# Kernel optimization log

Hardware: AMD Instinct MI355X
Metric: run time of the kernel (lower is better)

Reference implementation:

```python
import jax, jax.numpy as jnp
import numpy as np

EMBED_DIM = 1024
NUM_HEADS = 16
HEAD_DIM = EMBED_DIM // NUM_HEADS


def setup_inputs() -> dict:
    key = jax.random.key(0)
    ks = jax.random.split(key, 9)
    B, S, E = 4, 2048, EMBED_DIM
    # xavier_uniform bound for square [E, E] weights
    bound = float(np.sqrt(6.0 / (E + E)))
    def w(k):
        return jax.random.uniform(k, (E, E), jnp.float32, -bound, bound)
    return {
        "x": jax.random.normal(ks[0], (B, S, E), jnp.float32),
        "Wq": w(ks[1]), "bq": jnp.zeros((E,), jnp.float32),
        "Wk": w(ks[2]), "bk": jnp.zeros((E,), jnp.float32),
        "Wv": w(ks[3]), "bv": jnp.zeros((E,), jnp.float32),
        "Wo": w(ks[4]), "bo": jnp.zeros((E,), jnp.float32),
    }


def reference(x, Wq, bq, Wk, bk, Wv, bv, Wo, bo):
    B, S, E = x.shape
    H, D = NUM_HEADS, HEAD_DIM
    # Linear projections (torch Linear: x @ W.T + b)
    q = (x @ Wq.T + bq).reshape(B, S, H, D)
    k = (x @ Wk.T + bk).reshape(B, S, H, D)
    v = (x @ Wv.T + bv).reshape(B, S, H, D)
    # per-head scaled dot-product attention (vectorized over heads)
    scores = jnp.einsum("bqhd,bkhd->bhqk", q, k) / jnp.sqrt(jnp.float32(D))
    attn = jax.nn.softmax(scores, axis=-1)
    o = jnp.einsum("bhqk,bkhd->bqhd", attn, v).reshape(B, S, E)
    return o @ Wo.T + bo
```

## Files before the change

kernel.cpp:

```cpp
#include <hip/hip_runtime.h>
#include <stdint.h>

typedef unsigned short u16;
typedef short bf16x8 __attribute__((ext_vector_type(8)));
typedef float f32x4 __attribute__((ext_vector_type(4)));

#define B_ 4
#define S_ 2048
#define H_ 16
#define D_ 64
#define E_ 1024
#define M_ (B_ * S_)

static __device__ __forceinline__ u16 f2bf(float f) {
  uint32_t u = __builtin_bit_cast(uint32_t, f);
  u += 0x7fffu + ((u >> 16) & 1u);
  return (u16)(u >> 16);
}

static __device__ __forceinline__ void gld_lds16(const void* g, void* l) {
  __builtin_amdgcn_global_load_lds(
      (const __attribute__((address_space(1))) void*)(uintptr_t)g,
      (__attribute__((address_space(3))) void*)(uint32_t)(uintptr_t)l, 16, 0, 0);
}

template <int ctrl>
static __device__ __forceinline__ float dpp_mov(float x) {
  return __builtin_bit_cast(float,
      __builtin_amdgcn_update_dpp(0, __builtin_bit_cast(int, x), ctrl, 0xF, 0xF, true));
}
static __device__ __forceinline__ float rowsum16(float x) {
  x += dpp_mov<0xB1>(x);
  x += dpp_mov<0x4E>(x);
  x += dpp_mov<0x141>(x);
  x += dpp_mov<0x140>(x);
  return x;
}

__global__ __launch_bounds__(256) void cvt_f32_bf16(const float* __restrict__ in,
                                                    u16* __restrict__ out, int n) {
  int i = (blockIdx.x * 256 + threadIdx.x) * 8;
  if (i + 8 > n) return;
  float4 a = *(const float4*)(in + i);
  float4 b = *(const float4*)(in + i + 4);
  struct __align__(16) U8 { u16 h[8]; } u;
  u.h[0] = f2bf(a.x); u.h[1] = f2bf(a.y); u.h[2] = f2bf(a.z); u.h[3] = f2bf(a.w);
  u.h[4] = f2bf(b.x); u.h[5] = f2bf(b.y); u.h[6] = f2bf(b.z); u.h[7] = f2bf(b.w);
  *(U8*)(out + i) = u;
}

__device__ __forceinline__ void cstore(float* p, float v) { *p = v; }
__device__ __forceinline__ void cstore(u16* p, float v) { *p = f2bf(v); }

template <typename OutT>
static __device__ __forceinline__ void gemm_body(const u16* __restrict__ A,
                                                 const u16* __restrict__ W,
                                                 const float* __restrict__ bias,
                                                 OutT* __restrict__ C, int m0, int n0,
                                                 float scale) {
  __shared__ __align__(16) u16 As[128 * 32];
  __shared__ __align__(16) u16 Bs[128 * 32];
  const int tid = threadIdx.x;
  const int wave = tid >> 6, lane = tid & 63;
  const int col16 = lane & 15, quad = lane >> 4;
  const int wm = wave >> 1, wn = wave & 1;

  f32x4 acc[2][4] = {};

  const int r = tid >> 2;
  const int cofs = (tid & 3) * 8;
  const u16* ga = A + (size_t)(m0 + r) * E_ + cofs;
  const u16* gb = W + (size_t)(n0 + r) * E_ + cofs;
  u16* lA = As + wave * 512;
  u16* lB = Bs + wave * 512;

  for (int k0 = 0; k0 < E_; k0 += 32) {
    __syncthreads();
    gld_lds16(ga + k0, lA);
    gld_lds16(gb + k0, lB);
    asm volatile("s_waitcnt vmcnt(0)" ::: "memory");
    __syncthreads();

    bf16x8 af[2], bw[4];
#pragma unroll
    for (int mt = 0; mt < 2; mt++)
      af[mt] = *(const bf16x8*)&As[(wm * 32 + mt * 16 + col16) * 32 + quad * 8];
#pragma unroll
    for (int nt = 0; nt < 4; nt++)
      bw[nt] = *(const bf16x8*)&Bs[(wn * 64 + nt * 16 + col16) * 32 + quad * 8];
#pragma unroll
    for (int mt = 0; mt < 2; mt++)
#pragma unroll
      for (int nt = 0; nt < 4; nt++)
        acc[mt][nt] = __builtin_amdgcn_mfma_f32_16x16x32_bf16(af[mt], bw[nt], acc[mt][nt], 0, 0, 0);
  }

#pragma unroll
  for (int mt = 0; mt < 2; mt++) {
    int gr = m0 + wm * 32 + mt * 16 + quad * 4;
#pragma unroll
    for (int nt = 0; nt < 4; nt++) {
      int gc = n0 + wn * 64 + nt * 16 + col16;
      float bv = bias[gc];
#pragma unroll
      for (int e = 0; e < 4; e++)
        cstore(&C[(size_t)(gr + e) * E_ + gc], (acc[mt][nt][e] + bv) * scale);
    }
  }
}

__global__ __launch_bounds__(512) void gemm_qkv(const u16* __restrict__ xb,
                                                const u16* __restrict__ wq, const u16* __restrict__ wk,
                                                const u16* __restrict__ wv,
                                                const float* __restrict__ bq, const float* __restrict__ bk,
                                                const float* __restrict__ bv,
                                                u16* __restrict__ Qb, u16* __restrict__ Kb,
                                                u16* __restrict__ Vb) {
  const int mat = blockIdx.x >> 3;
  const int n0 = (blockIdx.x & 7) * 128;
  const u16* W = (mat == 0) ? wq : (mat == 1) ? wk : wv;
  const float* bias = (mat == 0) ? bq : (mat == 1) ? bk : bv;
  u16* C = (mat == 0) ? Qb : (mat == 1) ? Kb : Vb;
  const float scale = (mat == 0) ? (0.125f * 1.44269504f) : 1.0f;
  gemm_body<u16>(xb, W, bias, C, blockIdx.y * 128, n0, scale);
}

__global__ __launch_bounds__(512) void gemm_out(const u16* __restrict__ Ob,
                                                const u16* __restrict__ wob,
                                                const float* __restrict__ bo,
                                                float* __restrict__ out) {
  gemm_body<float>(Ob, wob, bo, out, blockIdx.y * 128, blockIdx.x * 128, 1.0f);
}

__global__ __launch_bounds__(256) void transpose_v(const u16* __restrict__ V,
                                                   u16* __restrict__ Vt) {
  __shared__ __align__(16) u16 tile[64 * 72];
  const int bid = blockIdx.x;
  const int sb = bid & 31, h = (bid >> 5) & 15, b = bid >> 9;
  const int tid = threadIdx.x;
  const int rr = tid >> 2;
  const int cc = (tid & 3) * 16;
  const u16* src = V + ((size_t)(b * S_ + sb * 64 + rr) * H_ + h) * D_ + cc;
  *(uint4*)&tile[rr * 72 + cc] = *(const uint4*)src;
  *(uint4*)&tile[rr * 72 + cc + 8] = *(const uint4*)(src + 8);
  __syncthreads();
  struct __align__(16) U16 { u16 h[16]; } vals;
#pragma unroll
  for (int j = 0; j < 16; j++) vals.h[j] = tile[(cc + j) * 72 + rr];
  u16* dst = Vt + ((size_t)((b * H_ + h) * D_ + rr)) * S_ + sb * 64 + cc;
  *(uint4*)dst = *(uint4*)&vals.h[0];
  *(uint4*)(dst + 8) = *(uint4*)&vals.h[8];
}

__global__ __launch_bounds__(256) void flash_attn(const u16* __restrict__ Q,
                                                  const u16* __restrict__ K,
                                                  const u16* __restrict__ Vt,
                                                  u16* __restrict__ O) {
  __shared__ __align__(16) u16 Ks[2][64 * 64];
  __shared__ __align__(16) u16 Vs[2][64 * 64];
  __shared__ __align__(16) u16 Ps[4][32 * 72];
  const int bid = blockIdx.x;
  const int qt = bid & 15, h = (bid >> 4) & 15, b = bid >> 8;
  const int tid = threadIdx.x;
  const int wave = tid >> 6, lane = tid & 63;
  const int col16 = lane & 15, quad = lane >> 4;

  bf16x8 qf[2][2];
  const int qrow = qt * 128 + wave * 32;
#pragma unroll
  for (int mt = 0; mt < 2; mt++) {
    const u16* qp = Q + ((size_t)(b * S_ + qrow + mt * 16 + col16) * H_ + h) * D_ + quad * 8;
    qf[mt][0] = *(const bf16x8*)qp;
    qf[mt][1] = *(const bf16x8*)(qp + 32);
  }

  f32x4 o_acc[2][4] = {};
  float l_i[2][4] = {};

  const int srow = tid >> 3;
  const int sgrp = (tid & 7) ^ (srow & 7);
  const u16* Kbase = K + ((size_t)(b * S_) * H_ + h) * D_;
  const u16* Vbase = Vt + ((size_t)(b * H_ + h) * D_) * S_;
  u16* Pw = &Ps[wave][0];

  auto stage = [&](int kb, int buf) {
#pragma unroll
    for (int i = 0; i < 2; i++) {
      gld_lds16(Kbase + (size_t)(kb * 64 + i * 32 + srow) * (H_ * D_) + sgrp * 8,
                &Ks[buf][i * 2048 + wave * 512]);
      gld_lds16(Vbase + (size_t)(i * 32 + srow) * S_ + kb * 64 + sgrp * 8,
                &Vs[buf][i * 2048 + wave * 512]);
    }
  };

  stage(0, 0);
  for (int kb = 0; kb < S_ / 64; kb++) {
    const int cur = kb & 1;
    asm volatile("s_waitcnt vmcnt(0)" ::: "memory");
    __syncthreads();
    if (kb + 1 < S_ / 64) stage(kb + 1, cur ^ 1);
    const u16* KsC = Ks[cur];
    const u16* VsC = Vs[cur];

    f32x4 sacc[2][4] = {};
#pragma unroll
    for (int ks = 0; ks < 2; ks++) {
      bf16x8 kf[4];
#pragma unroll
      for (int nt = 0; nt < 4; nt++)
        kf[nt] = *(const bf16x8*)&KsC[(nt * 16 + col16) * 64 +
                                      (((ks * 4 + quad) ^ (col16 & 7)) * 8)];
#pragma unroll
      for (int mt = 0; mt < 2; mt++)
#pragma unroll
        for (int nt = 0; nt < 4; nt++)
          sacc[mt][nt] = __builtin_amdgcn_mfma_f32_16x16x32_bf16(qf[mt][ks], kf[nt], sacc[mt][nt], 0, 0, 0);
    }

#pragma unroll
    for (int mt = 0; mt < 2; mt++) {
#pragma unroll
      for (int e = 0; e < 4; e++) {
        float p0 = __builtin_amdgcn_exp2f(sacc[mt][0][e]);
        float p1 = __builtin_amdgcn_exp2f(sacc[mt][1][e]);
        float p2 = __builtin_amdgcn_exp2f(sacc[mt][2][e]);
        float p3 = __builtin_amdgcn_exp2f(sacc[mt][3][e]);
        l_i[mt][e] += (p0 + p1) + (p2 + p3);
        const int r = mt * 16 + quad * 4 + e;
        const int ro = r * 72;
        const int cb = col16 + ((r & 8) ? 16 : 0);
        Pw[ro + (cb & 63)] = f2bf(p0);
        Pw[ro + ((cb + 16) & 63)] = f2bf(p1);
        Pw[ro + ((cb + 32) & 63)] = f2bf(p2);
        Pw[ro + ((cb + 48) & 63)] = f2bf(p3);
      }
    }
    asm volatile("s_waitcnt lgkmcnt(0)" ::: "memory");

#pragma unroll
    for (int ks = 0; ks < 2; ks++) {
      bf16x8 pf[2], vf[4];
#pragma unroll
      for (int mt = 0; mt < 2; mt++)
        pf[mt] = *(const bf16x8*)&Pw[(mt * 16 + col16) * 72 +
                                     (((ks * 4 + quad + ((col16 >> 3) << 1)) & 7) * 8)];
#pragma unroll
      for (int nt = 0; nt < 4; nt++)
        vf[nt] = *(const bf16x8*)&VsC[(nt * 16 + col16) * 64 +
                                      (((ks * 4 + quad) ^ (col16 & 7)) * 8)];
#pragma unroll
      for (int mt = 0; mt < 2; mt++)
#pragma unroll
        for (int nt = 0; nt < 4; nt++)
          o_acc[mt][nt] = __builtin_amdgcn_mfma_f32_16x16x32_bf16(pf[mt], vf[nt], o_acc[mt][nt], 0, 0, 0);
    }
  }

#pragma unroll
  for (int mt = 0; mt < 2; mt++) {
#pragma unroll
    for (int e = 0; e < 4; e++) {
      float inv = 1.f / rowsum16(l_i[mt][e]);
      int s = qrow + mt * 16 + quad * 4 + e;
#pragma unroll
      for (int nt = 0; nt < 4; nt++)
        O[((size_t)(b * S_ + s) * H_ + h) * D_ + nt * 16 + col16] =
            f2bf(o_acc[mt][nt][e] * inv);
    }
  }
}

extern "C" void kernel_launch(void* const* d_in, const int* in_sizes, int n_in,
                              void* d_out, int out_size, void* d_ws, size_t ws_size,
                              hipStream_t stream) {
  (void)in_sizes; (void)n_in; (void)out_size; (void)ws_size;
  const float* x  = (const float*)d_in[0];
  const float* Wq = (const float*)d_in[1];
  const float* bq = (const float*)d_in[2];
  const float* Wk = (const float*)d_in[3];
  const float* bk = (const float*)d_in[4];
  const float* Wv = (const float*)d_in[5];
  const float* bv = (const float*)d_in[6];
  const float* Wo = (const float*)d_in[7];
  const float* bo = (const float*)d_in[8];
  float* out = (float*)d_out;

  const size_t NX = (size_t)M_ * E_;
  const size_t NW = (size_t)E_ * E_;
  u16* xb  = (u16*)d_ws;
  u16* wqb = xb + NX;
  u16* wkb = wqb + NW;
  u16* wvb = wkb + NW;
  u16* wob = wvb + NW;
  u16* Qb  = wob + NW;
  u16* Kb  = Qb + NX;
  u16* Vb  = Kb + NX;
  u16* Vtb = Vb + NX;
  u16* Ob  = Vtb + NX;

  cvt_f32_bf16<<<NX / 2048, 256, 0, stream>>>(x, xb, (int)NX);
  cvt_f32_bf16<<<NW / 2048, 256, 0, stream>>>(Wq, wqb, (int)NW);
  cvt_f32_bf16<<<NW / 2048, 256, 0, stream>>>(Wk, wkb, (int)NW);
  cvt_f32_bf16<<<NW / 2048, 256, 0, stream>>>(Wv, wvb, (int)NW);
  cvt_f32_bf16<<<NW / 2048, 256, 0, stream>>>(Wo, wob, (int)NW);

  gemm_qkv<<<dim3(24, 64), 512, 0, stream>>>(xb, wqb, wkb, wvb, bq, bk, bv, Qb, Kb, Vb);
  transpose_v<<<B_ * H_ * (S_ / 64), 256, 0, stream>>>(Vb, Vtb);
  flash_attn<<<B_ * H_ * (S_ / 128), 256, 0, stream>>>(Qb, Kb, Vtb, Ob);
  gemm_out<<<dim3(8, 64), 512, 0, stream>>>(Ob, wob, bo, out);
}
```

Before: 314.8 us.

## Restructure GEMMs to 256 threads with K=64 swizzled tiles and fused V transpose

The GEMM kernel changes from 512 threads to 256 threads per 128x128 tile, so each wave now computes a 64x64 sub-tile with 16 MFMA accumulators. The K step doubles to 64 and LDS rows use an XOR swizzle to avoid bank conflicts. Operands are swapped so that epilogue stores write 4 contiguous values at once, and the V projection writes its transposed layout directly, which removes the separate transpose kernel and its memory round trip. Flash attention also switches to a cheaper round-half-up bf16 conversion for P. The trade-offs are more register pressure from the larger accumulator set and slightly different rounding.

New measurement: 303.2 us. -3.7%, faster.

```diff
diff --git a/kernel.cpp b/kernel.cpp
--- a/kernel.cpp
+++ b/kernel.cpp
@@ -16,6 +16,12 @@
   uint32_t u = __builtin_bit_cast(uint32_t, f);
   u += 0x7fffu + ((u >> 16) & 1u);
   return (u16)(u >> 16);
+}
+static __device__ __forceinline__ u16 hu16(float f) {
+  return (u16)((__builtin_bit_cast(uint32_t, f) + 0x8000u) >> 16);
+}
+static __device__ __forceinline__ uint32_t pack2bf(float a, float b) {
+  return (uint32_t)f2bf(a) | ((uint32_t)f2bf(b) << 16);
 }
 
 static __device__ __forceinline__ void gld_lds16(const void* g, void* l) {
@@ -49,107 +55,129 @@
   *(U8*)(out + i) = u;
 }
 
-__device__ __forceinline__ void cstore(float* p, float v) { *p = v; }
-__device__ __forceinline__ void cstore(u16* p, float v) { *p = f2bf(v); }
-
-template <typename OutT>
-static __device__ __forceinline__ void gemm_body(const u16* __restrict__ A,
-                                                 const u16* __restrict__ W,
-                                                 const float* __restrict__ bias,
-                                                 OutT* __restrict__ C, int m0, int n0,
-                                                 float scale) {
-  __shared__ __align__(16) u16 As[128 * 32];
-  __shared__ __align__(16) u16 Bs[128 * 32];
+template <int KIND, typename OutT>
+static __device__ __forceinline__ void gemm128(const u16* __restrict__ A,
+                                               const u16* __restrict__ W,
+                                               const float* __restrict__ bias,
+                                               OutT* __restrict__ C, int m0, int n0,
+                                               float scale, u16* As, u16* Bs) {
   const int tid = threadIdx.x;
   const int wave = tid >> 6, lane = tid & 63;
   const int col16 = lane & 15, quad = lane >> 4;
   const int wm = wave >> 1, wn = wave & 1;
 
-  f32x4 acc[2][4] = {};
-
-  const int r = tid >> 2;
-  const int cofs = (tid & 3) * 8;
-  const u16* ga = A + (size_t)(m0 + r) * E_ + cofs;
-  const u16* gb = W + (size_t)(n0 + r) * E_ + cofs;
+  f32x4 acc[4][4] = {};
+
+  const int r0 = tid >> 3;
+  const int sg8 = ((tid & 7) ^ (r0 & 7)) * 8;
+  const u16* ga = A + (size_t)(m0 + r0) * E_ + sg8;
+  const u16* gb = W + (size_t)(n0 + r0) * E_ + sg8;
   u16* lA = As + wave * 512;
   u16* lB = Bs + wave * 512;
 
-  for (int k0 = 0; k0 < E_; k0 += 32) {
+  for (int k0 = 0; k0 < E_; k0 += 64) {
     __syncthreads();
-    gld_lds16(ga + k0, lA);
-    gld_lds16(gb + k0, lB);
+#pragma unroll
+    for (int i = 0; i < 4; i++) {
+      gld_lds16(ga + (size_t)(i * 32) * E_ + k0, lA + i * 2048);
+      gld_lds16(gb + (size_t)(i * 32) * E_ + k0, lB + i * 2048);
+    }
     asm volatile("s_waitcnt vmcnt(0)" ::: "memory");
     __syncthreads();
 
-    bf16x8 af[2], bw[4];
-#pragma unroll
-    for (int mt = 0; mt < 2; mt++)
-      af[mt] = *(const bf16x8*)&As[(wm * 32 + mt * 16 + col16) * 32 + quad * 8];
+    bf16x8 af[4][2], bw[4][2];
+#pragma unroll
+    for (int mt = 0; mt < 4; mt++)
+#pragma unroll
+      for (int ks = 0; ks < 2; ks++)
+        af[mt][ks] = *(const bf16x8*)&As[(wm * 64 + mt * 16 + col16) * 64 +
+                                         (((ks * 4 + quad) ^ (col16 & 7)) * 8)];
 #pragma unroll
     for (int nt = 0; nt < 4; nt++)
-      bw[nt] = *(const bf16x8*)&Bs[(wn * 64 + nt * 16 + col16) * 32 + quad * 8];
-#pragma unroll
-    for (int mt = 0; mt < 2; mt++)
-#pragma unroll
-      for (int nt = 0; nt < 4; nt++)
-        acc[mt][nt] = __builtin_amdgcn_mfma_f32_16x16x32_bf16(af[mt], bw[nt], acc[mt][nt], 0, 0, 0);
-  }
-
-#pragma unroll
-  for (int mt = 0; mt < 2; mt++) {
-    int gr = m0 + wm * 32 + mt * 16 + quad * 4;
-#pragma unroll
-    for (int nt = 0; nt < 4; nt++) {
-      int gc = n0 + wn * 64 + nt * 16 + col16;
-      float bv = bias[gc];
-#pragma unroll
-      for (int e = 0; e < 4; e++)
-        cstore(&C[(size_t)(gr + e) * E_ + gc], (acc[mt][nt][e] + bv) * scale);
-    }
-  }
-}
-
-__global__ __launch_bounds__(512) void gemm_qkv(const u16* __restrict__ xb,
+#pragma unroll
+      for (int ks = 0; ks < 2; ks++)
+        bw[nt][ks] = *(const bf16x8*)&Bs[(wn * 64 + nt * 16 + col16) * 64 +
+                                         (((ks * 4 + quad) ^ (col16 & 7)) * 8)];
+#pragma unroll
+    for (int ks = 0; ks < 2; ks++)
+#pragma unroll
+      for (int a = 0; a < 4; a++)
+#pragma unroll
+        for (int b = 0; b < 4; b++) {
+          if constexpr (KIND == 2)
+            acc[a][b] = __builtin_amdgcn_mfma_f32_16x16x32_bf16(af[a][ks], bw[b][ks], acc[a][b], 0, 0, 0);
+          else
+            acc[a][b] = __builtin_amdgcn_mfma_f32_16x16x32_bf16(bw[a][ks], af[b][ks], acc[a][b], 0, 0, 0);
+        }
+  }
+
+  if constexpr (KIND == 2) {
+#pragma unroll
+    for (int a = 0; a < 4; a++) {
+      int t = m0 + wm * 64 + a * 16 + quad * 4;
+      int bb = t >> 11, s = t & (S_ - 1);
+#pragma unroll
+      for (int b = 0; b < 4; b++) {
+        int oc = n0 + wn * 64 + b * 16 + col16;
+        int h = oc >> 6, d = oc & 63;
+        float bv = bias[oc];
+        uint32_t lo = pack2bf(acc[a][b][0] + bv, acc[a][b][1] + bv);
+        uint32_t hi = pack2bf(acc[a][b][2] + bv, acc[a][b][3] + bv);
+        uint2 pk = {lo, hi};
+        *(uint2*)&C[(((size_t)(bb * H_ + h) * D_ + d) * S_) + s] = pk;
+      }
+    }
+  } else {
+#pragma unroll
+    for (int b = 0; b < 4; b++) {
+      int row = m0 + wm * 64 + b * 16 + col16;
+#pragma unroll
+      for (int a = 0; a < 4; a++) {
+        int nc = n0 + wn * 64 + a * 16 + quad * 4;
+        float4 bv = *(const float4*)&bias[nc];
+        float v0 = (acc[a][b][0] + bv.x) * scale;
+        float v1 = (acc[a][b][1] + bv.y) * scale;
+        float v2 = (acc[a][b][2] + bv.z) * scale;
+        float v3 = (acc[a][b][3] + bv.w) * scale;
+        if constexpr (KIND == 0) {
+          uint2 pk = {pack2bf(v0, v1), pack2bf(v2, v3)};
+          *(uint2*)&((u16*)C)[(size_t)row * E_ + nc] = pk;
+        } else {
+          float4 pk = {v0, v1, v2, v3};
+          *(float4*)&((float*)C)[(size_t)row * E_ + nc] = pk;
+        }
+      }
+    }
+  }
+}
+
+__global__ __launch_bounds__(256) void gemm_qkv(const u16* __restrict__ xb,
                                                 const u16* __restrict__ wq, const u16* __restrict__ wk,
                                                 const u16* __restrict__ wv,
                                                 const float* __restrict__ bq, const float* __restrict__ bk,
                                                 const float* __restrict__ bv,
                                                 u16* __restrict__ Qb, u16* __restrict__ Kb,
-                                                u16* __restrict__ Vb) {
+                                                u16* __restrict__ Vtb) {
+  __shared__ __align__(16) u16 As[128 * 64];
+  __shared__ __align__(16) u16 Bs[128 * 64];
   const int mat = blockIdx.x >> 3;
   const int n0 = (blockIdx.x & 7) * 128;
-  const u16* W = (mat == 0) ? wq : (mat == 1) ? wk : wv;
-  const float* bias = (mat == 0) ? bq : (mat == 1) ? bk : bv;
-  u16* C = (mat == 0) ? Qb : (mat == 1) ? Kb : Vb;
-  const float scale = (mat == 0) ? (0.125f * 1.44269504f) : 1.0f;
-  gemm_body<u16>(xb, W, bias, C, blockIdx.y * 128, n0, scale);
-}
-
-__global__ __launch_bounds__(512) void gemm_out(const u16* __restrict__ Ob,
+  const int m0 = blockIdx.y * 128;
+  if (mat == 0)
+    gemm128<0, u16>(xb, wq, bq, Qb, m0, n0, 0.125f * 1.44269504f, As, Bs);
+  else if (mat == 1)
+    gemm128<0, u16>(xb, wk, bk, Kb, m0, n0, 1.0f, As, Bs);
+  else
+    gemm128<2, u16>(xb, wv, bv, Vtb, m0, n0, 1.0f, As, Bs);
+}
+
+__global__ __launch_bounds__(256) void gemm_out(const u16* __restrict__ Ob,
                                                 const u16* __restrict__ wob,
                                                 const float* __restrict__ bo,
                                                 float* __restrict__ out) {
-  gemm_body<float>(Ob, wob, bo, out, blockIdx.y * 128, blockIdx.x * 128, 1.0f);
-}
-
-__global__ __launch_bounds__(256) void transpose_v(const u16* __restrict__ V,
-                                                   u16* __restrict__ Vt) {
-  __shared__ __align__(16) u16 tile[64 * 72];
-  const int bid = blockIdx.x;
-  const int sb = bid & 31, h = (bid >> 5) & 15, b = bid >> 9;
-  const int tid = threadIdx.x;
-  const int rr = tid >> 2;
-  const int cc = (tid & 3) * 16;
-  const u16* src = V + ((size_t)(b * S_ + sb * 64 + rr) * H_ + h) * D_ + cc;
-  *(uint4*)&tile[rr * 72 + cc] = *(const uint4*)src;
-  *(uint4*)&tile[rr * 72 + cc + 8] = *(const uint4*)(src + 8);
-  __syncthreads();
-  struct __align__(16) U16 { u16 h[16]; } vals;
-#pragma unroll
-  for (int j = 0; j < 16; j++) vals.h[j] = tile[(cc + j) * 72 + rr];
-  u16* dst = Vt + ((size_t)((b * H_ + h) * D_ + rr)) * S_ + sb * 64 + cc;
-  *(uint4*)dst = *(uint4*)&vals.h[0];
-  *(uint4*)(dst + 8) = *(uint4*)&vals.h[8];
+  __shared__ __align__(16) u16 As[128 * 64];
+  __shared__ __align__(16) u16 Bs[128 * 64];
+  gemm128<1, float>(Ob, wob, bo, out, blockIdx.y * 128, blockIdx.x * 128, 1.0f, As, Bs);
 }
 
 __global__ __launch_bounds__(256) void flash_attn(const u16* __restrict__ Q,
@@ -229,10 +257,10 @@
         const int r = mt * 16 + quad * 4 + e;
         const int ro = r * 72;
         const int cb = col16 + ((r & 8) ? 16 : 0);
-        Pw[ro + (cb & 63)] = f2bf(p0);
-        Pw[ro + ((cb + 16) & 63)] = f2bf(p1);
-        Pw[ro + ((cb + 32) & 63)] = f2bf(p2);
-        Pw[ro + ((cb + 48) & 63)] = f2bf(p3);
+        Pw[ro + (cb & 63)] = hu16(p0);
+        Pw[ro + ((cb + 16) & 63)] = hu16(p1);
+        Pw[ro + ((cb + 32) & 63)] = hu16(p2);
+        Pw[ro + ((cb + 48) & 63)] = hu16(p3);
       }
     }
     asm volatile("s_waitcnt lgkmcnt(0)" ::: "memory");
@@ -294,8 +322,7 @@
   u16* wob = wvb + NW;
   u16* Qb  = wob + NW;
   u16* Kb  = Qb + NX;
-  u16* Vb  = Kb + NX;
-  u16* Vtb = Vb + NX;
+  u16* Vtb = Kb + NX;
   u16* Ob  = Vtb + NX;
 
   cvt_f32_bf16<<<NX / 2048, 256, 0, stream>>>(x, xb, (int)NX);
@@ -304,8 +331,7 @@
   cvt_f32_bf16<<<NW / 2048, 256, 0, stream>>>(Wv, wvb, (int)NW);
   cvt_f32_bf16<<<NW / 2048, 256, 0, stream>>>(Wo, wob, (int)NW);
 
-  gemm_qkv<<<dim3(24, 64), 512, 0, stream>>>(xb, wqb, wkb, wvb, bq, bk, bv, Qb, Kb, Vb);
-  transpose_v<<<B_ * H_ * (S_ / 64), 256, 0, stream>>>(Vb, Vtb);
+  gemm_qkv<<<dim3(24, 64), 256, 0, stream>>>(xb, wqb, wkb, wvb, bq, bk, bv, Qb, Kb, Vtb);
   flash_attn<<<B_ * H_ * (S_ / 128), 256, 0, stream>>>(Qb, Kb, Vtb, Ob);
-  gemm_out<<<dim3(8, 64), 512, 0, stream>>>(Ob, wob, bo, out);
-}
+  gemm_out<<<dim3(8, 64), 256, 0, stream>>>(Ob, wob, bo, out);
+}
```
